# Kernel tuning notes

Hardware: AMD Instinct MI355X
Metric: run time of the kernel (lower is better)

## Reference

```python
import jax, jax.numpy as jnp
import numpy as np

B = 1
HEIGHT, WIDTH = 30, 52
HW = HEIGHT * WIDTH            # 1560
TQ = 2                         # query blocks -> Qtot = 3120
TK = 8                         # history blocks -> Ktot = 12480
KPQ = 2                        # selected kv blocks per query block
QTOT = TQ * HW
KTOT = TK * HW
HEADS = 12
DH = 128
DIM = HEADS * DH               # 1536, inner_dim == dim
EPS = 1e-5


def _rope_tables(S, D):
    # interleaved RoPE tables: freqs_cos[..., 0::2] == cos(ang), freqs_sin[..., 1::2] == sin(ang)
    inv_freq = 1.0 / (10000.0 ** (np.arange(0, D, 2, dtype=np.float32) / D))
    ang = np.arange(S, dtype=np.float32)[:, None] * inv_freq[None, :]      # [S, D/2]
    cos = np.repeat(np.cos(ang), 2, axis=-1)                                # [S, D]
    sin = np.repeat(np.sin(ang), 2, axis=-1)
    return (jnp.asarray(cos)[None, :, None, :], jnp.asarray(sin)[None, :, None, :])


def setup_inputs() -> dict:
    key = jax.random.key(0)
    ks = jax.random.split(key, 12)
    hidden_states = jax.random.normal(ks[0], (B, QTOT, DIM), jnp.float32)
    history_states = jax.random.normal(ks[1], (B, KTOT, DIM), jnp.float32)
    freqs_cos, freqs_sin = _rope_tables(QTOT, DH)
    freqs_cos_his, freqs_sin_his = _rope_tables(KTOT, DH)
    # first selected block always valid, second may be -1 (masked)
    sel0 = jax.random.randint(ks[2], (B, TQ, 1), 0, TK)
    sel1 = jax.random.randint(ks[3], (B, TQ, 1), -1, TK)
    sel_k_blocks = jnp.concatenate([sel0, sel1], axis=-1).astype(jnp.int32)  # [B, TQ, KPQ]
    s = 0.02
    Wq = jax.random.normal(ks[4], (DIM, DIM), jnp.float32) * s
    Wk = jax.random.normal(ks[5], (DIM, DIM), jnp.float32) * s
    Wv = jax.random.normal(ks[6], (DIM, DIM), jnp.float32) * s
    Wo = jax.random.normal(ks[7], (DIM, DIM), jnp.float32) * s
    bq = jnp.zeros((DIM,), jnp.float32)
    bk = jnp.zeros((DIM,), jnp.float32)
    bv = jnp.zeros((DIM,), jnp.float32)
    bo = jnp.zeros((DIM,), jnp.float32)
    gq = jnp.ones((DIM,), jnp.float32)
    gk = jnp.ones((DIM,), jnp.float32)
    return dict(hidden_states=hidden_states, history_states=history_states,
                freqs_cos=freqs_cos, freqs_sin=freqs_sin,
                freqs_cos_his=freqs_cos_his, freqs_sin_his=freqs_sin_his,
                sel_k_blocks=sel_k_blocks,
                Wq=Wq, bq=bq, Wk=Wk, bk=bk, Wv=Wv, bv=bv, Wo=Wo, bo=bo, gq=gq, gk=gk)


def _rmsnorm(x, g):
    return x * jax.lax.rsqrt(jnp.mean(x * x, axis=-1, keepdims=True) + EPS) * g


def _apply_rope(x, fc, fs):
    # x: [B, S, H, D]; fc/fs: [1, S, 1, D] interleaved tables
    x1 = x[..., 0::2]
    x2 = x[..., 1::2]
    cos = fc[..., 0::2]
    sin = fs[..., 1::2]
    even = x1 * cos - x2 * sin
    odd = x1 * sin + x2 * cos
    return jnp.stack([even, odd], axis=-1).reshape(x.shape)


def reference(hidden_states, history_states, freqs_cos, freqs_sin,
              freqs_cos_his, freqs_sin_his, sel_k_blocks,
              Wq, bq, Wk, bk, Wv, bv, Wo, bo, gq, gk):
    Bn, Qtot, _ = hidden_states.shape
    # projections + RMSNorm
    q = _rmsnorm(hidden_states @ Wq.T + bq, gq)
    k = _rmsnorm(history_states @ Wk.T + bk, gk)
    v = history_states @ Wv.T + bv
    q = q.reshape(Bn, QTOT, HEADS, DH)
    k = k.reshape(Bn, KTOT, HEADS, DH)
    v = v.reshape(Bn, KTOT, HEADS, DH)
    q = _apply_rope(q, freqs_cos, freqs_sin)
    k = _apply_rope(k, freqs_cos_his, freqs_sin_his)
    # [B, Hh, S, D] then blocked
    q_blk = q.transpose(0, 2, 1, 3).reshape(Bn, HEADS, TQ, HW, DH)
    k_blk = k.transpose(0, 2, 1, 3).reshape(Bn, HEADS, TK, HW, DH)
    v_blk = v.transpose(0, 2, 1, 3).reshape(Bn, HEADS, TK, HW, DH)
    # gather selected kv blocks (clamped indices; invalid masked later)
    idx = jnp.clip(sel_k_blocks, 0).reshape(Bn, TQ * KPQ)          # [B, TQ*KPQ]
    gather = jax.vmap(lambda kb, ib: kb[:, ib])                     # over batch
    k_sel = gather(k_blk, idx).reshape(Bn, HEADS, TQ, KPQ * HW, DH)
    v_sel = gather(v_blk, idx).reshape(Bn, HEADS, TQ, KPQ * HW, DH)
    scale = 1.0 / jnp.sqrt(jnp.float32(DH))
    scores = jnp.einsum('bhtqd,bhtkd->bhtqk', q_blk, k_sel) * scale  # [B,Hh,TQ,HW,KPQ*HW]
    valid = (sel_k_blocks >= 0)                                      # [B,TQ,KPQ]
    mask = jnp.repeat(valid, HW, axis=-1)[:, None, :, None, :]       # [B,1,TQ,1,KPQ*HW]
    scores = jnp.where(mask, scores, -jnp.inf)
    attnw = jax.nn.softmax(scores, axis=-1)
    out = jnp.einsum('bhtqk,bhtkd->bhtqd', attnw, v_sel)             # [B,Hh,TQ,HW,DH]
    out = out.reshape(Bn, HEADS, QTOT, DH).transpose(0, 2, 1, 3).reshape(Bn, QTOT, HEADS * DH)
    return out @ Wo.T + bo
```

## Files before the change

kernel.cpp:

```cpp
#include <hip/hip_runtime.h>

typedef unsigned short u16;
typedef __attribute__((ext_vector_type(4))) unsigned short u16x4;
typedef __attribute__((ext_vector_type(8))) unsigned short u16x8;
typedef __attribute__((ext_vector_type(4))) short s16x4;
typedef __attribute__((ext_vector_type(4))) float f32x4;
typedef __attribute__((ext_vector_type(8))) __bf16 bf16x8;

__device__ __forceinline__ u16 f2bf(float f) {
  union { float f; unsigned int u; } v; v.f = f;
  unsigned int u = v.u;
  unsigned int r = (u + 0x7fffu + ((u >> 16) & 1u)) >> 16;
  return (u16)r;
}
__device__ __forceinline__ u16 f2bf_hw(float f) {
  return __builtin_bit_cast(u16, (__bf16)f);
}
__device__ __forceinline__ float bf2f(u16 h) {
  union { unsigned int u; float f; } v; v.u = ((unsigned int)h) << 16;
  return v.f;
}
__device__ __forceinline__ f32x4 mfma16(u16x8 a, u16x8 b, f32x4 c) {
  return __builtin_amdgcn_mfma_f32_16x16x32_bf16(
      __builtin_bit_cast(bf16x8, a), __builtin_bit_cast(bf16x8, b), c, 0, 0, 0);
}
__device__ __forceinline__ f32x4 mfma16k16(u16x4 a, u16x4 b, f32x4 c) {
  return __builtin_amdgcn_mfma_f32_16x16x16bf16_1k(
      __builtin_bit_cast(s16x4, a), __builtin_bit_cast(s16x4, b), c, 0, 0, 0);
}
__device__ __forceinline__ void glds16(const void* g, void* l) {
  __builtin_amdgcn_global_load_lds((const __attribute__((address_space(1))) void*)g,
                                   (__attribute__((address_space(3))) void*)l, 16, 0, 0);
}
__device__ __forceinline__ int xcd_chunk(int bid, int nwg) {
  int xcd = bid & 7, idx = bid >> 3;
  int q = nwg >> 3, r = nwg & 7;
  int base = xcd < r ? xcd * (q + 1) : r * (q + 1) + (xcd - r) * q;
  return base + idx;
}
__device__ __forceinline__ int sel_mask(const int* __restrict__ sel) {
  int m = 0;
#pragma unroll
  for (int tt = 0; tt < 2; ++tt) {
    int a = sel[2 * tt];
    if (a < 0) a = 0;
    m |= 1 << a;
    int b = sel[2 * tt + 1];
    if (b >= 0) m |= 1 << b;
  }
  return m;
}

__global__ __launch_bounds__(256) void cvt_all(
    const float* __restrict__ hs, const float* __restrict__ his,
    const float* __restrict__ Wq, const float* __restrict__ Wk,
    const float* __restrict__ Wv, const float* __restrict__ Wo,
    u16* __restrict__ hsb, u16* __restrict__ hib,
    u16* __restrict__ wqb, u16* __restrict__ wkb,
    u16* __restrict__ wvb, u16* __restrict__ wob) {
  const int N0 = 1198080, N1 = 5990400, N2 = 6580224, N3 = 7170048, N4 = 7759872;
  int i = blockIdx.x * 256 + threadIdx.x;
  const float* s; u16* o; int base;
  if (i < N0)      { s = hs;  o = hsb; base = 0;  }
  else if (i < N1) { s = his; o = hib; base = N0; }
  else if (i < N2) { s = Wq;  o = wqb; base = N1; }
  else if (i < N3) { s = Wk;  o = wkb; base = N2; }
  else if (i < N4) { s = Wv;  o = wvb; base = N3; }
  else             { s = Wo;  o = wob; base = N4; }
  int j = i - base;
  float4 v = ((const float4*)s)[j];
  u16x4 r;
  r.x = f2bf(v.x); r.y = f2bf(v.y); r.z = f2bf(v.z); r.w = f2bf(v.w);
  ((u16x4*)o)[j] = r;
}

template <int OUT, int NBX>
__global__ __launch_bounds__(256, 2) void gemm_v2(
    const u16* __restrict__ A, const u16* __restrict__ W,
    const float* __restrict__ bias, void* __restrict__ Cp, int M) {
  const int K = 1536, N = 1536;
  __shared__ __align__(16) u16 gsm[17408];
  u16* As = gsm;
  u16* Bs = gsm + 8192;
  const int tid = threadIdx.x;
  const int lane = tid & 63, wid = tid >> 6;
  const int quad = lane >> 4, l15 = lane & 15;
  const int lg = xcd_chunk(blockIdx.x, gridDim.x);
  const int m0 = (lg / NBX) * 128, n0 = (lg % NBX) * 128;
  const int wm = (wid >> 1) * 64, wn = (wid & 1) * 64;
  f32x4 acc[4][4];
#pragma unroll
  for (int i = 0; i < 4; ++i)
#pragma unroll
    for (int j = 0; j < 4; ++j)
#pragma unroll
      for (int r = 0; r < 4; ++r) acc[i][j][r] = 0.f;

  const int r8 = lane >> 3, c8 = lane & 7;
  const int gch = c8 ^ r8;

  for (int k0 = 0; k0 < K; k0 += 64) {
#pragma unroll
    for (int inst = 0; inst < 4; ++inst) {
      int row = wid * 32 + inst * 8 + r8;
      glds16(A + ((size_t)(m0 + row) * K + k0 + gch * 8), As + (wid * 32 + inst * 8) * 64);
      glds16(W + ((size_t)(n0 + row) * K + k0 + gch * 8), Bs + (wid * 32 + inst * 8) * 64);
    }
    asm volatile("s_waitcnt vmcnt(0)" ::: "memory");
    __syncthreads();
#pragma unroll
    for (int ks = 0; ks < 2; ++ks) {
      u16x8 af[4], bfr[4];
#pragma unroll
      for (int i = 0; i < 4; ++i) {
        int row = wm + i * 16 + l15;
        af[i] = *(const u16x8*)&As[row * 64 + (((ks * 4 + quad) ^ (l15 & 7)) * 8)];
      }
#pragma unroll
      for (int j = 0; j < 4; ++j) {
        int row = wn + j * 16 + l15;
        bfr[j] = *(const u16x8*)&Bs[row * 64 + (((ks * 4 + quad) ^ (l15 & 7)) * 8)];
      }
#pragma unroll
      for (int i = 0; i < 4; ++i)
#pragma unroll
        for (int j = 0; j < 4; ++j) acc[i][j] = mfma16(af[i], bfr[j], acc[i][j]);
    }
    __syncthreads();
  }

#pragma unroll
  for (int i = 0; i < 4; ++i) {
    int row = m0 + wm + i * 16 + quad * 4;
#pragma unroll
    for (int j = 0; j < 4; ++j) {
      int col = n0 + wn + j * 16 + l15;
      float bc = bias[col];
#pragma unroll
      for (int r = 0; r < 4; ++r) {
        if (row + r < M) {
          float v = acc[i][j][r] + bc;
          if (OUT == 1)
            ((float*)Cp)[(size_t)(row + r) * N + col] = v;
          else
            ((u16*)Cp)[(size_t)(row + r) * N + col] = f2bf(v);
        }
      }
    }
  }
}

__global__ __launch_bounds__(256, 2) void gemm_kv(
    const u16* __restrict__ A, const u16* __restrict__ Wkv,
    const float* __restrict__ bk, const float* __restrict__ bv,
    u16* __restrict__ Ck, u16* __restrict__ Vt,
    const int* __restrict__ sel, int M, int ldt) {
  const int K = 1536;
  __shared__ __align__(16) u16 gsm[17408];
  u16* As = gsm;
  u16* Bs = gsm + 8192;
  const int tid = threadIdx.x;
  const int lane = tid & 63, wid = tid >> 6;
  const int quad = lane >> 4, l15 = lane & 15;
  const int lg = xcd_chunk(blockIdx.x, gridDim.x);
  const int qtr = lg / 588;
  const int rem = lg % 588;
  const int mi = rem / 6;
  const int m0 = ((mi * 25) % 98) * 128;
  const int n0 = (qtr * 6 + rem % 6) * 128;

  {
    int mask = sel_mask(sel);
    int tb0 = m0 / 1560;
    int tb1 = (m0 + 127) / 1560;
    if (!((mask >> tb0) & 1) && !((mask >> tb1) & 1)) return;
  }

  const int wm = (wid >> 1) * 64, wn = (wid & 1) * 64;
  f32x4 acc[4][4];
#pragma unroll
  for (int i = 0; i < 4; ++i)
#pragma unroll
    for (int j = 0; j < 4; ++j)
#pragma unroll
      for (int r = 0; r < 4; ++r) acc[i][j][r] = 0.f;

  const int r8 = lane >> 3, c8 = lane & 7;
  const int gch = c8 ^ r8;

  for (int k0 = 0; k0 < K; k0 += 64) {
#pragma unroll
    for (int inst = 0; inst < 4; ++inst) {
      int row = wid * 32 + inst * 8 + r8;
      glds16(A + ((size_t)(m0 + row) * K + k0 + gch * 8), As + (wid * 32 + inst * 8) * 64);
      glds16(Wkv + ((size_t)(n0 + row) * K + k0 + gch * 8), Bs + (wid * 32 + inst * 8) * 64);
    }
    asm volatile("s_waitcnt vmcnt(0)" ::: "memory");
    __syncthreads();
#pragma unroll
    for (int ks = 0; ks < 2; ++ks) {
      u16x8 af[4], bfr[4];
#pragma unroll
      for (int i = 0; i < 4; ++i) {
        int row = wm + i * 16 + l15;
        af[i] = *(const u16x8*)&As[row * 64 + (((ks * 4 + quad) ^ (l15 & 7)) * 8)];
      }
#pragma unroll
      for (int j = 0; j < 4; ++j) {
        int row = wn + j * 16 + l15;
        bfr[j] = *(const u16x8*)&Bs[row * 64 + (((ks * 4 + quad) ^ (l15 & 7)) * 8)];
      }
#pragma unroll
      for (int i = 0; i < 4; ++i)
#pragma unroll
        for (int j = 0; j < 4; ++j) acc[i][j] = mfma16(af[i], bfr[j], acc[i][j]);
    }
    __syncthreads();
  }

  if (n0 < 1536) {
#pragma unroll
    for (int i = 0; i < 4; ++i) {
      int row = m0 + wm + i * 16 + quad * 4;
#pragma unroll
      for (int j = 0; j < 4; ++j) {
        int col = n0 + wn + j * 16 + l15;
        float bc = bk[col];
#pragma unroll
        for (int r = 0; r < 4; ++r) {
          if (row + r < M)
            Ck[(size_t)(row + r) * 1536 + col] = f2bf(acc[i][j][r] + bc);
        }
      }
    }
  } else {
    const int n0v = n0 - 1536;
    u16* Ct = gsm;
#pragma unroll
    for (int i = 0; i < 4; ++i)
#pragma unroll
      for (int j = 0; j < 4; ++j) {
        int nloc = wn + j * 16 + l15;
        float bc = bv[n0v + nloc];
#pragma unroll
        for (int r = 0; r < 4; ++r) {
          int mloc = wm + i * 16 + quad * 4 + r;
          Ct[nloc * 136 + mloc] = f2bf(acc[i][j][r] + bc);
        }
      }
    __syncthreads();
    int n = tid >> 1, half = tid & 1;
#pragma unroll
    for (int e = 0; e < 8; ++e) {
      int mloc = half * 64 + e * 8;
      if (m0 + mloc < M) {
        u16x8 v = *(const u16x8*)&Ct[n * 136 + mloc];
        *(u16x8*)(Vt + (size_t)(n0v + n) * ldt + m0 + mloc) = v;
      }
    }
  }
}

__global__ __launch_bounds__(192) void norm_rope2(u16* __restrict__ X,
                                                  const float* __restrict__ g,
                                                  const float* __restrict__ fc,
                                                  const float* __restrict__ fs,
                                                  float oscale,
                                                  const int* __restrict__ sel) {
  const int DIMc = 1536;
  int row = blockIdx.x;
  if (sel) {
    int mask = sel_mask(sel);
    if (!((mask >> (row / 1560)) & 1)) return;
  }
  int tid = threadIdx.x;
  u16* xr = X + (size_t)row * DIMc + tid * 8;
  u16x8 v = *(const u16x8*)xr;
  float x[8];
  float ss = 0.f;
#pragma unroll
  for (int e = 0; e < 8; ++e) { x[e] = bf2f(v[e]); ss += x[e] * x[e]; }
#pragma unroll
  for (int m = 1; m < 64; m <<= 1) ss += __shfl_xor(ss, m);
  __shared__ float w3[3];
  if ((tid & 63) == 0) w3[tid >> 6] = ss;
  __syncthreads();
  float rs = rsqrtf((w3[0] + w3[1] + w3[2]) * (1.f / 1536.f) + 1e-5f);
  int dhb = (tid * 8) & 127;
  const float* fcr = fc + (size_t)row * 128 + dhb;
  const float* fsr = fs + (size_t)row * 128 + dhb;
  float4 c0 = *(const float4*)fcr, c1 = *(const float4*)(fcr + 4);
  float4 s0 = *(const float4*)fsr, s1 = *(const float4*)(fsr + 4);
  const float* gp = g + tid * 8;
  float4 g0 = *(const float4*)gp, g1 = *(const float4*)(gp + 4);
  float cosv[4] = {c0.x, c0.z, c1.x, c1.z};
  float sinv[4] = {s0.y, s0.w, s1.y, s1.w};
  float gv[8] = {g0.x, g0.y, g0.z, g0.w, g1.x, g1.y, g1.z, g1.w};
  u16x8 o;
#pragma unroll
  for (int p = 0; p < 4; ++p) {
    float a = x[2 * p] * rs * gv[2 * p];
    float b = x[2 * p + 1] * rs * gv[2 * p + 1];
    o[2 * p] = f2bf((a * cosv[p] - b * sinv[p]) * oscale);
    o[2 * p + 1] = f2bf((a * sinv[p] + b * cosv[p]) * oscale);
  }
  *(u16x8*)xr = o;
}

__global__ __launch_bounds__(256, 3) void attn13(
    const u16* __restrict__ Q, const u16* __restrict__ Kb,
    const u16* __restrict__ VT, const int* __restrict__ sel,
    float* __restrict__ Oacc, float* __restrict__ Lp) {
  const int HWc = 1560, DIMc = 1536, KTt = 12480, NT = 600;
  __shared__ __align__(16) u16 smem[16384];
  const int tid = threadIdx.x;
  const int lane = tid & 63, wid = tid >> 6;
  const int quad = lane >> 4, l15 = lane & 15;

  int bid = blockIdx.x;
  int xcd = bid & 7, idx = bid >> 3;
  int ug = idx / 13, mt = idx % 13;
  int u = xcd + 8 * ug;
  const int h = u / 6;
  const int slot = u % 6;

  const int nch0 = (sel[1] >= 0) ? 98 : 49;
  const int nch1 = (sel[3] >= 0) ? 98 : 49;
  const int ns0 = 6 * nch0 / (nch0 + nch1);
  const int t = (slot < ns0) ? 0 : 1;
  const int si = (slot < ns0) ? slot : slot - ns0;
  const int nseg = (slot < ns0) ? ns0 : 6 - ns0;
  const int m0 = mt * 128;
  const int g = h * 2 + t;

  int s0v = sel[2 * t];
  const int b0 = s0v > 0 ? s0v : 0;
  const int b1 = sel[2 * t + 1];
  const int nk = (b1 >= 0) ? 2 * HWc : HWc;
  const int nch = (b1 >= 0) ? 98 : 49;
  const int cpseg = (nch + nseg - 1) / nseg;
  const int c0 = si * cpseg;
  const int c1 = (c0 + cpseg < nch) ? c0 + cpseg : nch;

  u16x8 qf[2][4];
#pragma unroll
  for (int qt = 0; qt < 2; ++qt) {
    int qrow = m0 + wid * 32 + qt * 16 + l15;
    if (qrow > HWc - 1) qrow = HWc - 1;
    const u16* qp = Q + (size_t)(t * HWc + qrow) * DIMc + h * 128;
#pragma unroll
    for (int ks = 0; ks < 4; ++ks) qf[qt][ks] = *(const u16x8*)(qp + ks * 32 + quad * 8);
  }

  f32x4 oacc[2][8];
#pragma unroll
  for (int qt = 0; qt < 2; ++qt)
#pragma unroll
    for (int m = 0; m < 8; ++m)
#pragma unroll
      for (int r = 0; r < 4; ++r) oacc[qt][m][r] = 0.f;
  float lp[2] = {0.f, 0.f};

  auto stage = [&](int kc, int buf) {
    u16* Ks = smem + buf * 4096;
    u16* Vt = smem + 8192 + buf * 4096;
#pragma unroll
    for (int n = 0; n < 2; ++n) {
      int kl = wid * 8 + n * 4 + (lane >> 4);
      int gc = (lane & 15) ^ (kl & 15);
      int kg = kc + kl;
      if (kg >= nk) kg = 0;
      int big = kg >= HWc;
      int tok = (big ? b1 : b0) * HWc + kg - (big ? HWc : 0);
      glds16(Kb + ((size_t)tok * DIMc + h * 128 + gc * 8), Ks + (wid * 8 + n * 4) * 128);
    }
#pragma unroll
    for (int n = 0; n < 2; ++n) {
      int dl = wid * 32 + n * 16 + (lane >> 2);
      int gc = (lane & 3) ^ (dl & 3) ^ ((dl >> 2) & 3);
      int tg = kc + gc * 8;
      if (tg >= nk) tg = 0;
      int big = tg >= HWc;
      int tok = (big ? b1 : b0) * HWc + tg - (big ? HWc : 0);
      glds16(VT + ((size_t)(h * 128 + dl) * KTt + tok), Vt + (wid * 32 + n * 16) * 32);
    }
  };

  if (c0 < c1) stage(c0 * 32, 0);

  for (int c = c0; c < c1; ++c) {
    const int buf = (c - c0) & 1;
    u16* Ks = smem + buf * 4096;
    u16* Vt = smem + 8192 + buf * 4096;
    asm volatile("s_waitcnt vmcnt(0)\n\ts_barrier" ::: "memory");
    if (c + 1 < c1) stage((c + 1) * 32, buf ^ 1);

    f32x4 s[2][2];
#pragma unroll
    for (int gg = 0; gg < 2; ++gg)
#pragma unroll
      for (int qt = 0; qt < 2; ++qt)
#pragma unroll
        for (int r = 0; r < 4; ++r) s[gg][qt][r] = 0.f;
#pragma unroll
    for (int ks = 0; ks < 4; ++ks)
#pragma unroll
      for (int gg = 0; gg < 2; ++gg) {
        u16x8 ka = *(const u16x8*)&Ks[(gg * 16 + l15) * 128 + (((ks * 4 + quad) ^ l15) * 8)];
#pragma unroll
        for (int qt = 0; qt < 2; ++qt) s[gg][qt] = mfma16(ka, qf[qt][ks], s[gg][qt]);
      }

    float p[2][2][4];
#pragma unroll
    for (int gg = 0; gg < 2; ++gg)
#pragma unroll
      for (int qt = 0; qt < 2; ++qt)
#pragma unroll
        for (int r = 0; r < 4; ++r) p[gg][qt][r] = exp2f(s[gg][qt][r]);
    if ((c + 1) * 32 > nk) {
#pragma unroll
      for (int gg = 0; gg < 2; ++gg)
#pragma unroll
        for (int r = 0; r < 4; ++r) {
          bool bad = c * 32 + gg * 16 + quad * 4 + r >= nk;
          if (bad) {
#pragma unroll
            for (int qt = 0; qt < 2; ++qt) p[gg][qt][r] = 0.f;
          }
        }
    }
    u16x4 pb[2][2];
#pragma unroll
    for (int gg = 0; gg < 2; ++gg)
#pragma unroll
      for (int qt = 0; qt < 2; ++qt)
#pragma unroll
        for (int r = 0; r < 4; ++r) {
          lp[qt] += p[gg][qt][r];
          pb[gg][qt][r] = f2bf_hw(p[gg][qt][r]);
        }

#pragma unroll
    for (int m = 0; m < 8; ++m) {
      int d = m * 16 + l15;
#pragma unroll
      for (int gg = 0; gg < 2; ++gg) {
        int sl = (gg * 2 + (quad >> 1)) ^ (d & 3) ^ ((d >> 2) & 3);
        u16x4 va = *(const u16x4*)&Vt[d * 32 + sl * 8 + (quad & 1) * 4];
#pragma unroll
        for (int qt = 0; qt < 2; ++qt) oacc[qt][m] = mfma16k16(va, pb[gg][qt], oacc[qt][m]);
      }
    }
  }

#pragma unroll
  for (int qt = 0; qt < 2; ++qt) {
    lp[qt] += __shfl_xor(lp[qt], 16);
    lp[qt] += __shfl_xor(lp[qt], 32);
  }
#pragma unroll
  for (int qt = 0; qt < 2; ++qt) {
    int qrow0 = m0 + wid * 32 + qt * 16;
    if (qrow0 < HWc) {
      size_t sb = ((size_t)si * NT + g * 25 + (qrow0 >> 6)) * 64 + (qrow0 & 63);
      if (lane < 16 && qrow0 + lane < HWc) Lp[sb + lane] = lp[qt];
      if (qrow0 + l15 < HWc) {
#pragma unroll
        for (int m = 0; m < 8; ++m)
          *(f32x4*)&Oacc[(sb + l15) * 128 + m * 16 + quad * 4] = oacc[qt][m];
      }
    }
  }
}

__global__ __launch_bounds__(256) void attn_norm(const float* __restrict__ Oacc,
                                                 const float* __restrict__ Lp,
                                                 const int* __restrict__ sel,
                                                 u16* __restrict__ O) {
  const int HWc = 1560, DIMc = 1536, NT = 600;
  int tile = blockIdx.x;
  int g = tile / 25, mt = tile % 25;
  int h = g >> 1, t = g & 1;
  int m0 = mt * 64;
  int tid = threadIdx.x;
  const int nch0 = (sel[1] >= 0) ? 98 : 49;
  const int nch1 = (sel[3] >= 0) ? 98 : 49;
  const int ns0 = 6 * nch0 / (nch0 + nch1);
  const int nseg = (t == 0) ? ns0 : 6 - ns0;
#pragma unroll
  for (int e = 0; e < 8; ++e) {
    int idx = e * 256 + tid;
    int qloc = idx >> 5;
    int d4 = (idx & 31) * 4;
    int q = m0 + qloc;
    if (q < HWc) {
      f32x4 a = {0.f, 0.f, 0.f, 0.f};
      float l = 0.f;
      for (int s = 0; s < nseg; ++s) {
        const size_t sbase = ((size_t)s * NT + tile) * 64 + qloc;
        f32x4 v = *(const f32x4*)&Oacc[sbase * 128 + d4];
#pragma unroll
        for (int r = 0; r < 4; ++r) a[r] += v[r];
        l += Lp[sbase];
      }
      float linv = 1.f / l;
      u16x4 o;
#pragma unroll
      for (int r = 0; r < 4; ++r) o[r] = f2bf(a[r] * linv);
      *(u16x4*)(O + (size_t)(t * HWc + q) * DIMc + h * 128 + d4) = o;
    }
  }
}

extern "C" void kernel_launch(void* const* d_in, const int* in_sizes, int n_in,
                              void* d_out, int out_size, void* d_ws, size_t ws_size,
                              hipStream_t stream) {
  const float* hs  = (const float*)d_in[0];
  const float* his = (const float*)d_in[1];
  const float* fc  = (const float*)d_in[2];
  const float* fs  = (const float*)d_in[3];
  const float* fch = (const float*)d_in[4];
  const float* fsh = (const float*)d_in[5];
  const int*   sel = (const int*)d_in[6];
  const float* Wq  = (const float*)d_in[7];
  const float* bq  = (const float*)d_in[8];
  const float* Wk  = (const float*)d_in[9];
  const float* bk  = (const float*)d_in[10];
  const float* Wv  = (const float*)d_in[11];
  const float* bv  = (const float*)d_in[12];
  const float* Wo  = (const float*)d_in[13];
  const float* bo  = (const float*)d_in[14];
  const float* gq  = (const float*)d_in[15];
  const float* gk  = (const float*)d_in[16];

  const int QT = 3120, KT = 12480, DIMc = 1536;
  u16* p = (u16*)d_ws;
  u16* qb  = p; p += (size_t)QT * DIMc;
  u16* kb2 = p; p += (size_t)KT * DIMc;
  u16* vt  = p; p += (size_t)DIMc * KT;
  u16* ab  = p; p += (size_t)QT * DIMc;
  u16* wob = p; p += (size_t)DIMc * DIMc;
  u16* scratch = p;
  u16* hsb = scratch;
  u16* hib = hsb + (size_t)QT * DIMc;
  u16* wqb = hib + (size_t)KT * DIMc;
  u16* wkb = wqb + (size_t)DIMc * DIMc;
  u16* wvb = wkb + (size_t)DIMc * DIMc;
  float* oaccb = (float*)scratch;
  float* lpb   = oaccb + (size_t)4 * 600 * 64 * 128;

  cvt_all<<<dim3(32616), 256, 0, stream>>>(hs, his, Wq, Wk, Wv, Wo,
                                           hsb, hib, wqb, wkb, wvb, wob);

  gemm_v2<0, 12><<<dim3(300), 256, 0, stream>>>(hsb, wqb, bq, qb, QT);
  gemm_kv<<<dim3(2352), 256, 0, stream>>>(hib, wkb, bk, bv, kb2, vt, sel, KT, KT);

  const float qscale = (float)(0.08838834764831845 * 1.4426950408889634);
  norm_rope2<<<dim3(QT), 192, 0, stream>>>(qb, gq, fc, fs, qscale, nullptr);
  norm_rope2<<<dim3(KT), 192, 0, stream>>>(kb2, gk, fch, fsh, 1.0f, sel);

  attn13<<<dim3(936), 256, 0, stream>>>(qb, kb2, vt, sel, oaccb, lpb);
  attn_norm<<<dim3(600), 256, 0, stream>>>(oaccb, lpb, sel, ab);

  gemm_v2<1, 12><<<dim3(300), 256, 0, stream>>>(ab, wob, bo, d_out, QT);
}
```

Before: 460.2 us.

## Merge Q and KV projections and norm launches, skip converting unselected history rows

```diff
diff --git a/kernel.cpp b/kernel.cpp
--- a/kernel.cpp
+++ b/kernel.cpp
@@ -57,7 +57,8 @@
     const float* __restrict__ Wv, const float* __restrict__ Wo,
     u16* __restrict__ hsb, u16* __restrict__ hib,
     u16* __restrict__ wqb, u16* __restrict__ wkb,
-    u16* __restrict__ wvb, u16* __restrict__ wob) {
+    u16* __restrict__ wvb, u16* __restrict__ wob,
+    const int* __restrict__ sel) {
   const int N0 = 1198080, N1 = 5990400, N2 = 6580224, N3 = 7170048, N4 = 7759872;
   int i = blockIdx.x * 256 + threadIdx.x;
   const float* s; u16* o; int base;
@@ -68,6 +69,10 @@
   else if (i < N4) { s = Wv;  o = wvb; base = N3; }
   else             { s = Wo;  o = wob; base = N4; }
   int j = i - base;
+  if (base == N0) {
+    int row = j / 384;
+    if (!((sel_mask(sel) >> (row / 1560)) & 1)) return;
+  }
   float4 v = ((const float4*)s)[j];
   u16x4 r;
   r.x = f2bf(v.x); r.y = f2bf(v.y); r.z = f2bf(v.z); r.w = f2bf(v.w);
@@ -150,11 +155,13 @@
   }
 }
 
-__global__ __launch_bounds__(256, 2) void gemm_kv(
-    const u16* __restrict__ A, const u16* __restrict__ Wkv,
-    const float* __restrict__ bk, const float* __restrict__ bv,
-    u16* __restrict__ Ck, u16* __restrict__ Vt,
-    const int* __restrict__ sel, int M, int ldt) {
+__global__ __launch_bounds__(256, 2) void gemm_qkv(
+    const u16* __restrict__ Aq, const u16* __restrict__ Akv,
+    const u16* __restrict__ Wqp, const u16* __restrict__ Wkv,
+    const float* __restrict__ bq, const float* __restrict__ bk,
+    const float* __restrict__ bv,
+    u16* __restrict__ Cq, u16* __restrict__ Ck, u16* __restrict__ Vt,
+    const int* __restrict__ sel, int ldt) {
   const int K = 1536;
   __shared__ __align__(16) u16 gsm[17408];
   u16* As = gsm;
@@ -163,17 +170,28 @@
   const int lane = tid & 63, wid = tid >> 6;
   const int quad = lane >> 4, l15 = lane & 15;
   const int lg = xcd_chunk(blockIdx.x, gridDim.x);
-  const int qtr = lg / 588;
-  const int rem = lg % 588;
-  const int mi = rem / 6;
-  const int m0 = ((mi * 25) % 98) * 128;
-  const int n0 = (qtr * 6 + rem % 6) * 128;
-
-  {
-    int mask = sel_mask(sel);
-    int tb0 = m0 / 1560;
-    int tb1 = (m0 + 127) / 1560;
-    if (!((mask >> tb0) & 1) && !((mask >> tb1) & 1)) return;
+
+  const u16 *A, *W;
+  const float* bias;
+  u16* out;
+  int m0, n0, M, vmode;
+  if (lg < 300) {
+    A = Aq; W = Wqp; bias = bq; out = Cq;
+    m0 = (lg / 12) * 128; n0 = (lg % 12) * 128; M = 3120; vmode = 0;
+  } else {
+    int L2 = lg - 300;
+    int qtr = L2 / 588, rem = L2 % 588;
+    int mi = rem / 6;
+    m0 = ((mi * 25) % 98) * 128;
+    n0 = (qtr * 6 + rem % 6) * 128;
+    {
+      int mask = sel_mask(sel);
+      int tb0 = m0 / 1560, tb1 = (m0 + 127) / 1560;
+      if (!((mask >> tb0) & 1) && !((mask >> tb1) & 1)) return;
+    }
+    A = Akv; W = Wkv; M = 12480;
+    if (n0 < 1536) { bias = bk; out = Ck; vmode = 0; }
+    else { bias = bv; out = nullptr; vmode = 1; }
   }
 
   const int wm = (wid >> 1) * 64, wn = (wid & 1) * 64;
@@ -193,7 +211,7 @@
     for (int inst = 0; inst < 4; ++inst) {
       int row = wid * 32 + inst * 8 + r8;
       glds16(A + ((size_t)(m0 + row) * K + k0 + gch * 8), As + (wid * 32 + inst * 8) * 64);
-      glds16(Wkv + ((size_t)(n0 + row) * K + k0 + gch * 8), Bs + (wid * 32 + inst * 8) * 64);
+      glds16(W + ((size_t)(n0 + row) * K + k0 + gch * 8), Bs + (wid * 32 + inst * 8) * 64);
     }
     asm volatile("s_waitcnt vmcnt(0)" ::: "memory");
     __syncthreads();
@@ -218,18 +236,18 @@
     __syncthreads();
   }
 
-  if (n0 < 1536) {
+  if (vmode == 0) {
 #pragma unroll
     for (int i = 0; i < 4; ++i) {
       int row = m0 + wm + i * 16 + quad * 4;
 #pragma unroll
       for (int j = 0; j < 4; ++j) {
         int col = n0 + wn + j * 16 + l15;
-        float bc = bk[col];
+        float bc = bias[col];
 #pragma unroll
         for (int r = 0; r < 4; ++r) {
           if (row + r < M)
-            Ck[(size_t)(row + r) * 1536 + col] = f2bf(acc[i][j][r] + bc);
+            out[(size_t)(row + r) * 1536 + col] = f2bf(acc[i][j][r] + bc);
         }
       }
     }
@@ -241,7 +259,7 @@
 #pragma unroll
       for (int j = 0; j < 4; ++j) {
         int nloc = wn + j * 16 + l15;
-        float bc = bv[n0v + nloc];
+        float bc = bias[n0v + nloc];
 #pragma unroll
         for (int r = 0; r < 4; ++r) {
           int mloc = wm + i * 16 + quad * 4 + r;
@@ -261,17 +279,24 @@
   }
 }
 
-__global__ __launch_bounds__(192) void norm_rope2(u16* __restrict__ X,
-                                                  const float* __restrict__ g,
-                                                  const float* __restrict__ fc,
-                                                  const float* __restrict__ fs,
-                                                  float oscale,
-                                                  const int* __restrict__ sel) {
+__global__ __launch_bounds__(192) void norm_rope_all(
+    u16* __restrict__ Xq, u16* __restrict__ Xk,
+    const float* __restrict__ gq, const float* __restrict__ gk,
+    const float* __restrict__ fc, const float* __restrict__ fs,
+    const float* __restrict__ fch, const float* __restrict__ fsh,
+    float qscale, const int* __restrict__ sel) {
   const int DIMc = 1536;
-  int row = blockIdx.x;
-  if (sel) {
-    int mask = sel_mask(sel);
-    if (!((mask >> (row / 1560)) & 1)) return;
+  int bidr = blockIdx.x;
+  u16* X;
+  const float *g, *fcp, *fsp;
+  float oscale;
+  int row;
+  if (bidr < 3120) {
+    X = Xq; g = gq; fcp = fc; fsp = fs; oscale = qscale; row = bidr;
+  } else {
+    row = bidr - 3120;
+    if (!((sel_mask(sel) >> (row / 1560)) & 1)) return;
+    X = Xk; g = gk; fcp = fch; fsp = fsh; oscale = 1.0f;
   }
   int tid = threadIdx.x;
   u16* xr = X + (size_t)row * DIMc + tid * 8;
@@ -287,8 +312,8 @@
   __syncthreads();
   float rs = rsqrtf((w3[0] + w3[1] + w3[2]) * (1.f / 1536.f) + 1e-5f);
   int dhb = (tid * 8) & 127;
-  const float* fcr = fc + (size_t)row * 128 + dhb;
-  const float* fsr = fs + (size_t)row * 128 + dhb;
+  const float* fcr = fcp + (size_t)row * 128 + dhb;
+  const float* fsr = fsp + (size_t)row * 128 + dhb;
   float4 c0 = *(const float4*)fcr, c1 = *(const float4*)(fcr + 4);
   float4 s0 = *(const float4*)fsr, s1 = *(const float4*)(fsr + 4);
   const float* gp = g + tid * 8;
@@ -551,14 +576,14 @@
   float* lpb   = oaccb + (size_t)4 * 600 * 64 * 128;
 
   cvt_all<<<dim3(32616), 256, 0, stream>>>(hs, his, Wq, Wk, Wv, Wo,
-                                           hsb, hib, wqb, wkb, wvb, wob);
-
-  gemm_v2<0, 12><<<dim3(300), 256, 0, stream>>>(hsb, wqb, bq, qb, QT);
-  gemm_kv<<<dim3(2352), 256, 0, stream>>>(hib, wkb, bk, bv, kb2, vt, sel, KT, KT);
+                                           hsb, hib, wqb, wkb, wvb, wob, sel);
+
+  gemm_qkv<<<dim3(2652), 256, 0, stream>>>(hsb, hib, wqb, wkb, bq, bk, bv,
+                                           qb, kb2, vt, sel, KT);
 
   const float qscale = (float)(0.08838834764831845 * 1.4426950408889634);
-  norm_rope2<<<dim3(QT), 192, 0, stream>>>(qb, gq, fc, fs, qscale, nullptr);
-  norm_rope2<<<dim3(KT), 192, 0, stream>>>(kb2, gk, fch, fsh, 1.0f, sel);
+  norm_rope_all<<<dim3(QT + KT), 192, 0, stream>>>(qb, kb2, gq, gk, fc, fs, fch, fsh,
+                                                   qscale, sel);
 
   attn13<<<dim3(936), 256, 0, stream>>>(qb, kb2, vt, sel, oaccb, lpb);
   attn_norm<<<dim3(600), 256, 0, stream>>>(oaccb, lpb, sel, ab);
```

Measured after the change: 453.2 us. About the same (-1.5%).
